# Performance work log

Measured on AMD Instinct MI355X. Metric: run time of the kernel, lower is better.

Reference implementation:

```python
import jax, jax.numpy as jnp
import numpy as np

N = 128   # n_features == out_dim (required by the Christoffel permutes)
H = 256   # MLP hidden width of forward_func
B = 16    # batch size (state_batch is [2B, N])
EPS_G = 1e-4
EPS_DG = 1e-6
EPS_V = 1e-6


def setup_inputs() -> dict:
    key = jax.random.key(0)
    ks = jax.random.split(key, 6)
    return {
        "t": jax.random.uniform(ks[0], (), dtype=jnp.float32),
        "state_batch": jax.random.normal(ks[1], (2 * B, N), dtype=jnp.float32) * 0.1,
        "x0_batch": jax.random.normal(ks[2], (B, N), dtype=jnp.float32),
        "x1_batch": jax.random.normal(ks[3], (B, N), dtype=jnp.float32),
        "W1": jax.random.normal(ks[4], (N, H), dtype=jnp.float32) / np.float32(np.sqrt(N)),
        "b1": jnp.zeros((H,), dtype=jnp.float32),
        "W2": jax.random.normal(ks[5], (H, N), dtype=jnp.float32) / np.float32(np.sqrt(H)),
        "b2": jnp.zeros((N,), dtype=jnp.float32),
    }


def reference(t, state_batch, x0_batch, x1_batch, W1, b1, W2, b2):
    def f(x):  # forward_func, per-sample: [N] -> [N]
        return jnp.tanh(x @ W1 + b1) @ W2 + b2

    def metric(x):  # G(x) = J J^T + 1e-4 I, per-sample: [N] -> [N, N]
        J = jax.jacrev(f)(x)                      # [N, N], matches per-output grad loop
        return J @ J.T + EPS_G * jnp.eye(N, dtype=x.dtype)

    deviation, dev_velocity = jnp.split(state_batch, 2, axis=0)  # each [B, N]
    window = 4.0 * t * (1.0 - t)
    # x along the perturbed straight path
    x = x0_batch + t * (x1_batch - x0_batch) + window * deviation  # [B, N]

    # dG[b, i, j, k] = dG_ij/dx_k -- replaces the out_dim^2 autograd.grad loop
    dG = jax.vmap(jax.jacfwd(metric))(x)  # [B, N, N, N]
    nrm = jnp.sqrt(jnp.sum(dG * dG, axis=(1, 2, 3), keepdims=True))
    dG = dG / (nrm + EPS_DG)

    # Christoffel-like symbols
    Gamma = 0.5 * (dG + jnp.transpose(dG, (0, 2, 1, 3)) - jnp.transpose(dG, (0, 3, 1, 2)))
    a = -jnp.einsum('bijk,bj,bk->bi', Gamma, dev_velocity, dev_velocity)
    a = a / (jnp.linalg.norm(dev_velocity, axis=1, keepdims=True) + EPS_V)

    restoration = -0.1 * deviation
    return jnp.concatenate([dev_velocity, a + restoration], axis=0)  # [2B, N]
```

## Files before the change

### kernel.cpp

```cpp
#include <hip/hip_runtime.h>
#include <math.h>


static constexpr int OFF_W2T  = 0;
static constexpr int OFF_S    = 32768;
static constexpr int OFF_Q    = 98304;
static constexpr int OFF_D    = 163840;
static constexpr int OFF_C    = 167936;
static constexpr int OFF_UV   = 172032;
static constexpr int OFF_AV   = 176128;
static constexpr int OFF_VN   = 180224;
static constexpr int OFF_SUM  = 180240;
static constexpr int OFF_CNT  = 180256;
static constexpr int OFF_PT   = 180288;
static constexpr int OFF_PN   = 704576;

__global__ __launch_bounds__(256) void k_stage1(const float* __restrict__ tptr,
                                                const float* __restrict__ state,
                                                const float* __restrict__ x0,
                                                const float* __restrict__ x1,
                                                const float* __restrict__ W1,
                                                const float* __restrict__ b1,
                                                const float* __restrict__ W2,
                                                float* __restrict__ ws,
                                                float* __restrict__ out) {
    __shared__ __align__(16) float smem[2 * 32 * 34];
    int blk = blockIdx.x;
    int tid = threadIdx.x;

    if (blk < 64) {
        float* Ai = smem;
        float* Aj = smem + 1088;
        int m0 = (blk >> 3) * 32, n0 = (blk & 7) * 32;
        int lx = tid & 31, lr = tid >> 5;
        int tx = tid & 15, ty = tid >> 4;
        float a00 = 0, a01 = 0, a10 = 0, a11 = 0;
        for (int kc = 0; kc < 128; kc += 32) {
            #pragma unroll
            for (int i = 0; i < 4; ++i) {
                int k = lr + 8 * i;
                Ai[k * 34 + lx] = W1[(kc + k) * 256 + m0 + lx];
                Aj[k * 34 + lx] = W1[(kc + k) * 256 + n0 + lx];
            }
            __syncthreads();
            #pragma unroll
            for (int k = 0; k < 32; ++k) {
                float2 a = *(const float2*)&Ai[k * 34 + 2 * ty];
                float2 b = *(const float2*)&Aj[k * 34 + 2 * tx];
                a00 += a.x * b.x; a01 += a.x * b.y;
                a10 += a.y * b.x; a11 += a.y * b.y;
            }
            __syncthreads();
        }
        float* S = ws + OFF_S;
        int m = m0 + 2 * ty, n = n0 + 2 * tx;
        S[m * 256 + n]           = a00;
        S[m * 256 + n + 1]       = a01;
        S[(m + 1) * 256 + n]     = a10;
        S[(m + 1) * 256 + n + 1] = a11;
    } else if (blk < 128) {
        float* Xi = smem;
        float* Xj = smem + 1088;
        int bq = blk - 64;
        int m0 = (bq >> 3) * 32, n0 = (bq & 7) * 32;
        int lx = tid & 31, lr = tid >> 5;
        int tx = tid & 15, ty = tid >> 4;
        float a00 = 0, a01 = 0, a10 = 0, a11 = 0;
        for (int kc = 0; kc < 128; kc += 32) {
            #pragma unroll
            for (int i = 0; i < 4; ++i) {
                Xi[lx * 34 + lr + 8 * i] = W2[(m0 + lr + 8 * i) * 128 + kc + lx];
                Xj[lx * 34 + lr + 8 * i] = W2[(n0 + lr + 8 * i) * 128 + kc + lx];
            }
            __syncthreads();
            #pragma unroll
            for (int k = 0; k < 32; ++k) {
                float2 a = *(const float2*)&Xi[k * 34 + 2 * ty];
                float2 b = *(const float2*)&Xj[k * 34 + 2 * tx];
                a00 += a.x * b.x; a01 += a.x * b.y;
                a10 += a.y * b.x; a11 += a.y * b.y;
            }
            __syncthreads();
        }
        float* Q = ws + OFF_Q;
        int m = m0 + 2 * ty, n = n0 + 2 * tx;
        Q[m * 256 + n]           = a00;
        Q[m * 256 + n + 1]       = a01;
        Q[(m + 1) * 256 + n]     = a10;
        Q[(m + 1) * 256 + n + 1] = a11;
    } else if (blk < 160) {
        float* tile = smem;
        int b2 = blk - 128;
        int c0 = (b2 & 3) * 32, r0 = (b2 >> 2) * 32;
        int tx = tid & 31, ty = tid >> 5;
        #pragma unroll
        for (int i = 0; i < 32; i += 8)
            tile[(ty + i) * 33 + tx] = W2[(r0 + ty + i) * 128 + c0 + tx];
        __syncthreads();
        float* W2T = ws + OFF_W2T;
        #pragma unroll
        for (int i = 0; i < 32; i += 8)
            W2T[(c0 + ty + i) * 256 + r0 + tx] = tile[tx * 33 + ty + i];
    } else {
        int b = blk - 160;
        float* xs  = smem;
        float* vs  = smem + 128;
        float* red = smem + 256;
        float t = tptr[0];
        float w = 4.f * t * (1.f - t);
        if (tid == 0) {
            ws[OFF_SUM + b] = 0.f;
            ((int*)(ws + OFF_CNT))[b] = 0;
        }
        if (tid < 128) {
            float dev = state[b * 128 + tid];
            float v   = state[(16 + b) * 128 + tid];
            float xv  = x0[b * 128 + tid] + t * (x1[b * 128 + tid] - x0[b * 128 + tid]) + w * dev;
            xs[tid] = xv;
            vs[tid] = v;
            out[b * 128 + tid] = v;
            red[tid] = v * v;
        }
        __syncthreads();
        for (int s = 64; s > 0; s >>= 1) {
            if (tid < s) red[tid] += red[tid + s];
            __syncthreads();
        }
        if (tid == 0) ws[OFF_VN + b] = sqrtf(red[0]);

        int m = tid;
        float h = b1[m], uvm = 0.f;
        #pragma unroll 8
        for (int k = 0; k < 128; ++k) {
            float wv = W1[k * 256 + m];
            h   += xs[k] * wv;
            uvm += vs[k] * wv;
        }
        float z  = tanhf(h);
        float dd = 1.f - z * z;
        float cc = -2.f * z * dd;
        const float4* w2r = (const float4*)&W2[m * 128];
        const float4* vs4 = (const float4*)vs;
        float avm = 0.f;
        #pragma unroll 8
        for (int j4 = 0; j4 < 32; ++j4) {
            float4 ww = w2r[j4];
            float4 vv = vs4[j4];
            avm += ww.x * vv.x + ww.y * vv.y + ww.z * vv.z + ww.w * vv.w;
        }
        ws[OFF_D  + b * 256 + m] = dd;
        ws[OFF_C  + b * 256 + m] = cc;
        ws[OFF_UV + b * 256 + m] = uvm;
        ws[OFF_AV + b * 256 + m] = avm;
    }
}

__global__ __launch_bounds__(256) void k_pmat3(const float* __restrict__ Smat,
                                               const float* __restrict__ dall,
                                               const float* __restrict__ W2,
                                               float* __restrict__ PT,
                                               float* __restrict__ Pn) {
    __shared__ __align__(16) float ST[32 * 36];
    __shared__ __align__(16) float YT[32 * 68];
    int b = blockIdx.z, mt = blockIdx.y, jt = blockIdx.x;
    int m0 = mt * 32, j0 = jt * 64;
    const float* dvec = dall + b * 256;
    int tid = threadIdx.x;
    int n = tid >> 3, c4 = (tid & 7) * 4;
    int ty = tid >> 5, tx = tid & 31;
    float acc[4][2] = {};
    for (int nc = 0; nc < 256; nc += 32) {
        *(float4*)&ST[n * 36 + c4] = *(const float4*)&Smat[(nc + n) * 256 + m0 + c4];
        float dn = dvec[nc + n];
        #pragma unroll
        for (int i = 0; i < 2; ++i) {
            int col = c4 + 32 * i;
            float4 wv = *(const float4*)&W2[(nc + n) * 128 + j0 + col];
            wv.x *= dn; wv.y *= dn; wv.z *= dn; wv.w *= dn;
            *(float4*)&YT[n * 68 + col] = wv;
        }
        __syncthreads();
        #pragma unroll 8
        for (int k = 0; k < 32; ++k) {
            float4 a  = *(const float4*)&ST[k * 36 + 4 * ty];
            float2 bb = *(const float2*)&YT[k * 68 + 2 * tx];
            acc[0][0] += a.x * bb.x; acc[0][1] += a.x * bb.y;
            acc[1][0] += a.y * bb.x; acc[1][1] += a.y * bb.y;
            acc[2][0] += a.z * bb.x; acc[2][1] += a.z * bb.y;
            acc[3][0] += a.w * bb.x; acc[3][1] += a.w * bb.y;
        }
        __syncthreads();
    }
    float* ptb = PT + b * 32768;
    float* pnb = Pn + b * 32768;
    #pragma unroll
    for (int jj = 0; jj < 2; ++jj) {
        float4 v = make_float4(acc[0][jj], acc[1][jj], acc[2][jj], acc[3][jj]);
        *(float4*)&ptb[(j0 + 2 * tx + jj) * 256 + m0 + 4 * ty] = v;
    }
    #pragma unroll
    for (int ii = 0; ii < 4; ++ii) {
        float2 v = make_float2(acc[ii][0], acc[ii][1]);
        *(float2*)&pnb[(m0 + 4 * ty + ii) * 128 + j0 + 2 * tx] = v;
    }
}

__global__ __launch_bounds__(256) void k_fnorm3(const float* __restrict__ PT,
                                                const float* __restrict__ Pn,
                                                const float* __restrict__ W2T,
                                                const float* __restrict__ Smat,
                                                const float* __restrict__ Qmat,
                                                const float* __restrict__ state,
                                                const float* __restrict__ W2,
                                                float* __restrict__ ws,
                                                float* __restrict__ out) {
    __shared__ __align__(16) float lds[16384];
    __shared__ int lastflag;
    __shared__ float snrm;
    float* PiT = lds;
    float* PjT = lds + 4096;
    float* WiT = lds + 8192;
    float* WjT = lds + 12288;
    int b = blockIdx.y;
    int idx = blockIdx.x;
    int tj = 0;
    while ((tj + 1) * (tj + 2) / 2 <= idx) ++tj;
    int ti = idx - tj * (tj + 1) / 2;
    int mi0 = ti * 32, mj0 = tj * 32;
    int tid = threadIdx.x;
    const float* ptb = PT + b * 32768;
    int jr = tid >> 3, jc4 = (tid & 7) * 4;
    #pragma unroll
    for (int it = 0; it < 4; ++it) {
        int j = jr + 32 * it;
        *(float4*)&PiT[j * 32 + jc4] = *(const float4*)&ptb[j * 256 + mi0 + jc4];
        *(float4*)&PjT[j * 32 + jc4] = *(const float4*)&ptb[j * 256 + mj0 + jc4];
        *(float4*)&WiT[j * 32 + jc4] = *(const float4*)&W2T[j * 256 + mi0 + jc4];
        *(float4*)&WjT[j * 32 + jc4] = *(const float4*)&W2T[j * 256 + mj0 + jc4];
    }
    __syncthreads();
    int w = tid >> 6, s = tid & 63;
    int ty = s >> 3, tx = s & 7;
    float r[4][4] = {}, f[4][4] = {}, g[4][4] = {};
    int jbase = 32 * w;
    #pragma unroll 4
    for (int jj = 0; jj < 32; ++jj) {
        int j = jbase + jj;
        float4 pi4 = *(const float4*)&PiT[j * 32 + 4 * ty];
        float4 pj4 = *(const float4*)&PjT[j * 32 + 4 * tx];
        float4 wi4 = *(const float4*)&WiT[j * 32 + 4 * ty];
        float4 wj4 = *(const float4*)&WjT[j * 32 + 4 * tx];
        float pi[4] = {pi4.x, pi4.y, pi4.z, pi4.w};
        float pj[4] = {pj4.x, pj4.y, pj4.z, pj4.w};
        float wi[4] = {wi4.x, wi4.y, wi4.z, wi4.w};
        float wj[4] = {wj4.x, wj4.y, wj4.z, wj4.w};
        #pragma unroll
        for (int ii = 0; ii < 4; ++ii)
            #pragma unroll
            for (int kk = 0; kk < 4; ++kk) {
                r[ii][kk] += pi[ii] * pj[kk];
                f[ii][kk] += pi[ii] * wj[kk];
                g[ii][kk] += pj[kk] * wi[ii];
            }
    }
    __syncthreads();
    {
        float* scr = lds;
        int base = tid * 48;
        #pragma unroll
        for (int ii = 0; ii < 4; ++ii)
            #pragma unroll
            for (int kk = 0; kk < 4; ++kk) {
                scr[base + ii * 4 + kk]      = r[ii][kk];
                scr[base + 16 + ii * 4 + kk] = f[ii][kk];
                scr[base + 32 + ii * 4 + kk] = g[ii][kk];
            }
    }
    __syncthreads();
    if (tid < 64) {
        const float* scr = lds;
        float tr[16], tf[16], tg[16];
        #pragma unroll
        for (int k = 0; k < 16; ++k) {
            tr[k] = scr[tid * 48 + k]      + scr[(tid + 64) * 48 + k]
                  + scr[(tid + 128) * 48 + k] + scr[(tid + 192) * 48 + k];
            tf[k] = scr[tid * 48 + 16 + k]      + scr[(tid + 64) * 48 + 16 + k]
                  + scr[(tid + 128) * 48 + 16 + k] + scr[(tid + 192) * 48 + 16 + k];
            tg[k] = scr[tid * 48 + 32 + k]      + scr[(tid + 64) * 48 + 32 + k]
                  + scr[(tid + 128) * 48 + 32 + k] + scr[(tid + 192) * 48 + 32 + k];
        }
        const float* cb = ws + OFF_C + b * 256;
        int mi = mi0 + 4 * (tid >> 3), mj = mj0 + 4 * (tid & 7);
        float4 ce4 = *(const float4*)&cb[mj];
        float ce[4] = {ce4.x, ce4.y, ce4.z, ce4.w};
        float sum = 0.f;
        #pragma unroll
        for (int ii = 0; ii < 4; ++ii) {
            float ci = cb[mi + ii];
            float4 S4 = *(const float4*)&Smat[(mi + ii) * 256 + mj];
            float4 Q4 = *(const float4*)&Qmat[(mi + ii) * 256 + mj];
            float Sv[4] = {S4.x, S4.y, S4.z, S4.w};
            float Qv[4] = {Q4.x, Q4.y, Q4.z, Q4.w};
            #pragma unroll
            for (int kk = 0; kk < 4; ++kk)
                sum += ci * ce[kk] * Sv[kk] * (Qv[kk] * tr[ii * 4 + kk] + tf[ii * 4 + kk] * tg[ii * 4 + kk]);
        }
        if (ti < tj) sum *= 2.f;
        #pragma unroll
        for (int off = 32; off > 0; off >>= 1)
            sum += __shfl_down(sum, off);
        if (tid == 0) {
            atomicAdd(&ws[OFF_SUM + b], sum);
            __threadfence();
            int old = atomicAdd(((int*)(ws + OFF_CNT)) + b, 1);
            lastflag = (old == 35) ? 1 : 0;
        }
    }
    __syncthreads();
    if (!lastflag) return;

    float* vs  = lds;
    float* g1  = lds + 128;
    float* g2  = lds + 384;
    float* red = lds + 640;
    if (tid == 0) {
        float tot = atomicAdd(&ws[OFF_SUM + b], 0.0f);
        snrm = sqrtf(fmaxf(2.f * tot, 0.f));
    }
    if (tid < 128) vs[tid] = state[(16 + b) * 128 + tid];
    __syncthreads();
    const float* pnb = Pn + b * 32768;
    int m = tid;
    float pv = 0.f;
    #pragma unroll 8
    for (int j = 0; j < 128; ++j)
        pv += ptb[j * 256 + m] * vs[j];
    float cc  = ws[OFF_C  + b * 256 + m];
    float uvm = ws[OFF_UV + b * 256 + m];
    float avm = ws[OFF_AV + b * 256 + m];
    g1[m] = cc * pv  * uvm;
    g2[m] = cc * avm * uvm;
    __syncthreads();
    int i = tid & 127, half = tid >> 7;
    int mmlo = half * 128;
    float raw = 0.f;
    #pragma unroll 8
    for (int mm = mmlo; mm < mmlo + 128; ++mm)
        raw += W2[mm * 128 + i] * g1[mm] + pnb[mm * 128 + i] * g2[mm];
    red[tid] = raw;
    __syncthreads();
    if (tid < 128) {
        float rawt = red[tid] + red[tid + 128];
        float vn = ws[OFF_VN + b];
        float a  = -0.5f * rawt / ((snrm + 1e-6f) * (vn + 1e-6f));
        out[(16 + b) * 128 + tid] = a - 0.1f * state[b * 128 + tid];
    }
}

extern "C" void kernel_launch(void* const* d_in, const int* in_sizes, int n_in,
                              void* d_out, int out_size, void* d_ws, size_t ws_size,
                              hipStream_t stream) {
    (void)in_sizes; (void)n_in; (void)out_size; (void)ws_size;
    const float* t     = (const float*)d_in[0];
    const float* state = (const float*)d_in[1];
    const float* x0    = (const float*)d_in[2];
    const float* x1    = (const float*)d_in[3];
    const float* W1    = (const float*)d_in[4];
    const float* b1    = (const float*)d_in[5];
    const float* W2    = (const float*)d_in[6];
    float* out = (float*)d_out;
    float* ws  = (float*)d_ws;

    k_stage1<<<176, 256, 0, stream>>>(t, state, x0, x1, W1, b1, W2, ws, out);
    k_pmat3<<<dim3(2, 8, 16), 256, 0, stream>>>(ws + OFF_S, ws + OFF_D, W2,
                                                ws + OFF_PT, ws + OFF_PN);
    k_fnorm3<<<dim3(36, 16), 256, 0, stream>>>(ws + OFF_PT, ws + OFF_PN, ws + OFF_W2T,
                                               ws + OFF_S, ws + OFF_Q,
                                               state, W2, ws, out);
}
```

Measured before the change: 129.0 us.

## Fuse three kernels into one cooperative persistent kernel with grid syncs

Merges the stage1, pmat and fnorm kernels into a single cooperative kernel of 256 blocks that separates phases with grid.sync. The final per-batch reduction now runs after a grid barrier instead of using atomic counters and a last-block flag. The aim is to remove launch gaps and the inter-kernel boundaries. In exchange, grid barriers cost time, the fnorm tiles are spread over a fixed grid through a strided loop, and all blocks carry the larger LDS footprint. The scratch stride was also padded from 48 to 49 to reduce LDS bank conflicts.

Result: slower. 218.5 us (+69.4%).

```diff
diff --git a/kernel.cpp b/kernel.cpp
--- a/kernel.cpp
+++ b/kernel.cpp
@@ -1,5 +1,8 @@
 #include <hip/hip_runtime.h>
+#include <hip/hip_cooperative_groups.h>
 #include <math.h>
+
+namespace cg = cooperative_groups;
 
 
 static constexpr int OFF_W2T  = 0;
@@ -11,26 +14,27 @@
 static constexpr int OFF_AV   = 176128;
 static constexpr int OFF_VN   = 180224;
 static constexpr int OFF_SUM  = 180240;
-static constexpr int OFF_CNT  = 180256;
-static constexpr int OFF_PT   = 180288;
-static constexpr int OFF_PN   = 704576;
-
-__global__ __launch_bounds__(256) void k_stage1(const float* __restrict__ tptr,
+static constexpr int OFF_PT   = 180256;
+static constexpr int OFF_PN   = OFF_PT + 16 * 32768;
+
+__global__ __launch_bounds__(256, 1) void k_all(const float* __restrict__ tptr,
                                                 const float* __restrict__ state,
                                                 const float* __restrict__ x0,
                                                 const float* __restrict__ x1,
                                                 const float* __restrict__ W1,
                                                 const float* __restrict__ b1,
                                                 const float* __restrict__ W2,
-                                                float* __restrict__ ws,
-                                                float* __restrict__ out) {
-    __shared__ __align__(16) float smem[2 * 32 * 34];
+                                                float* ws,
+                                                float* out) {
+    __shared__ __align__(16) float lds[16384];
+    __shared__ float snrm;
+    cg::grid_group grid = cg::this_grid();
     int blk = blockIdx.x;
     int tid = threadIdx.x;
 
     if (blk < 64) {
-        float* Ai = smem;
-        float* Aj = smem + 1088;
+        float* Ai = lds;
+        float* Aj = lds + 1088;
         int m0 = (blk >> 3) * 32, n0 = (blk & 7) * 32;
         int lx = tid & 31, lr = tid >> 5;
         int tx = tid & 15, ty = tid >> 4;
@@ -59,8 +63,8 @@
         S[(m + 1) * 256 + n]     = a10;
         S[(m + 1) * 256 + n + 1] = a11;
     } else if (blk < 128) {
-        float* Xi = smem;
-        float* Xj = smem + 1088;
+        float* Xi = lds;
+        float* Xj = lds + 1088;
         int bq = blk - 64;
         int m0 = (bq >> 3) * 32, n0 = (bq & 7) * 32;
         int lx = tid & 31, lr = tid >> 5;
@@ -88,30 +92,14 @@
         Q[m * 256 + n + 1]       = a01;
         Q[(m + 1) * 256 + n]     = a10;
         Q[(m + 1) * 256 + n + 1] = a11;
-    } else if (blk < 160) {
-        float* tile = smem;
-        int b2 = blk - 128;
-        int c0 = (b2 & 3) * 32, r0 = (b2 >> 2) * 32;
-        int tx = tid & 31, ty = tid >> 5;
-        #pragma unroll
-        for (int i = 0; i < 32; i += 8)
-            tile[(ty + i) * 33 + tx] = W2[(r0 + ty + i) * 128 + c0 + tx];
-        __syncthreads();
-        float* W2T = ws + OFF_W2T;
-        #pragma unroll
-        for (int i = 0; i < 32; i += 8)
-            W2T[(c0 + ty + i) * 256 + r0 + tx] = tile[tx * 33 + ty + i];
-    } else {
-        int b = blk - 160;
-        float* xs  = smem;
-        float* vs  = smem + 128;
-        float* red = smem + 256;
+    } else if (blk < 144) {
+        int b = blk - 128;
+        float* xs  = lds;
+        float* vs  = lds + 128;
+        float* red = lds + 256;
         float t = tptr[0];
         float w = 4.f * t * (1.f - t);
-        if (tid == 0) {
-            ws[OFF_SUM + b] = 0.f;
-            ((int*)(ws + OFF_CNT))[b] = 0;
-        }
+        if (tid == 0) ws[OFF_SUM + b] = 0.f;
         if (tid < 128) {
             float dev = state[b * 128 + tid];
             float v   = state[(16 + b) * 128 + tid];
@@ -152,208 +140,212 @@
         ws[OFF_C  + b * 256 + m] = cc;
         ws[OFF_UV + b * 256 + m] = uvm;
         ws[OFF_AV + b * 256 + m] = avm;
+    } else if (blk < 160) {
+        float* tile = lds;
+        int tx = tid & 31, ty = tid >> 5;
+        for (int tt = 0; tt < 2; ++tt) {
+            int t2 = (blk - 144) * 2 + tt;
+            int c0 = (t2 & 3) * 32, r0 = (t2 >> 2) * 32;
+            #pragma unroll
+            for (int i = 0; i < 32; i += 8)
+                tile[(ty + i) * 33 + tx] = W2[(r0 + ty + i) * 128 + c0 + tx];
+            __syncthreads();
+            float* W2T = ws + OFF_W2T;
+            #pragma unroll
+            for (int i = 0; i < 32; i += 8)
+                W2T[(c0 + ty + i) * 256 + r0 + tx] = tile[tx * 33 + ty + i];
+            __syncthreads();
+        }
     }
-}
-
-__global__ __launch_bounds__(256) void k_pmat3(const float* __restrict__ Smat,
-                                               const float* __restrict__ dall,
-                                               const float* __restrict__ W2,
-                                               float* __restrict__ PT,
-                                               float* __restrict__ Pn) {
-    __shared__ __align__(16) float ST[32 * 36];
-    __shared__ __align__(16) float YT[32 * 68];
-    int b = blockIdx.z, mt = blockIdx.y, jt = blockIdx.x;
-    int m0 = mt * 32, j0 = jt * 64;
-    const float* dvec = dall + b * 256;
-    int tid = threadIdx.x;
-    int n = tid >> 3, c4 = (tid & 7) * 4;
-    int ty = tid >> 5, tx = tid & 31;
-    float acc[4][2] = {};
-    for (int nc = 0; nc < 256; nc += 32) {
-        *(float4*)&ST[n * 36 + c4] = *(const float4*)&Smat[(nc + n) * 256 + m0 + c4];
-        float dn = dvec[nc + n];
+    grid.sync();
+
+    {
+        float* ST = lds;
+        float* YT = lds + 32 * 36;
+        int b = blk >> 4, rem = blk & 15;
+        int mt = rem >> 1, jt = rem & 1;
+        int m0 = mt * 32, j0 = jt * 64;
+        const float* dvec = ws + OFF_D + b * 256;
+        const float* Smat = ws + OFF_S;
+        int n = tid >> 3, c4 = (tid & 7) * 4;
+        int ty = tid >> 5, tx = tid & 31;
+        float acc[4][2] = {};
+        for (int nc = 0; nc < 256; nc += 32) {
+            *(float4*)&ST[n * 36 + c4] = *(const float4*)&Smat[(nc + n) * 256 + m0 + c4];
+            float dn = dvec[nc + n];
+            #pragma unroll
+            for (int i = 0; i < 2; ++i) {
+                int col = c4 + 32 * i;
+                float4 wv = *(const float4*)&W2[(nc + n) * 128 + j0 + col];
+                wv.x *= dn; wv.y *= dn; wv.z *= dn; wv.w *= dn;
+                *(float4*)&YT[n * 68 + col] = wv;
+            }
+            __syncthreads();
+            #pragma unroll 8
+            for (int k = 0; k < 32; ++k) {
+                float4 a  = *(const float4*)&ST[k * 36 + 4 * ty];
+                float2 bb = *(const float2*)&YT[k * 68 + 2 * tx];
+                acc[0][0] += a.x * bb.x; acc[0][1] += a.x * bb.y;
+                acc[1][0] += a.y * bb.x; acc[1][1] += a.y * bb.y;
+                acc[2][0] += a.z * bb.x; acc[2][1] += a.z * bb.y;
+                acc[3][0] += a.w * bb.x; acc[3][1] += a.w * bb.y;
+            }
+            __syncthreads();
+        }
+        float* ptb = ws + OFF_PT + b * 32768;
+        float* pnb = ws + OFF_PN + b * 32768;
         #pragma unroll
-        for (int i = 0; i < 2; ++i) {
-            int col = c4 + 32 * i;
-            float4 wv = *(const float4*)&W2[(nc + n) * 128 + j0 + col];
-            wv.x *= dn; wv.y *= dn; wv.z *= dn; wv.w *= dn;
-            *(float4*)&YT[n * 68 + col] = wv;
-        }
-        __syncthreads();
-        #pragma unroll 8
-        for (int k = 0; k < 32; ++k) {
-            float4 a  = *(const float4*)&ST[k * 36 + 4 * ty];
-            float2 bb = *(const float2*)&YT[k * 68 + 2 * tx];
-            acc[0][0] += a.x * bb.x; acc[0][1] += a.x * bb.y;
-            acc[1][0] += a.y * bb.x; acc[1][1] += a.y * bb.y;
-            acc[2][0] += a.z * bb.x; acc[2][1] += a.z * bb.y;
-            acc[3][0] += a.w * bb.x; acc[3][1] += a.w * bb.y;
-        }
-        __syncthreads();
-    }
-    float* ptb = PT + b * 32768;
-    float* pnb = Pn + b * 32768;
-    #pragma unroll
-    for (int jj = 0; jj < 2; ++jj) {
-        float4 v = make_float4(acc[0][jj], acc[1][jj], acc[2][jj], acc[3][jj]);
-        *(float4*)&ptb[(j0 + 2 * tx + jj) * 256 + m0 + 4 * ty] = v;
-    }
-    #pragma unroll
-    for (int ii = 0; ii < 4; ++ii) {
-        float2 v = make_float2(acc[ii][0], acc[ii][1]);
-        *(float2*)&pnb[(m0 + 4 * ty + ii) * 128 + j0 + 2 * tx] = v;
-    }
-}
-
-__global__ __launch_bounds__(256) void k_fnorm3(const float* __restrict__ PT,
-                                                const float* __restrict__ Pn,
-                                                const float* __restrict__ W2T,
-                                                const float* __restrict__ Smat,
-                                                const float* __restrict__ Qmat,
-                                                const float* __restrict__ state,
-                                                const float* __restrict__ W2,
-                                                float* __restrict__ ws,
-                                                float* __restrict__ out) {
-    __shared__ __align__(16) float lds[16384];
-    __shared__ int lastflag;
-    __shared__ float snrm;
-    float* PiT = lds;
-    float* PjT = lds + 4096;
-    float* WiT = lds + 8192;
-    float* WjT = lds + 12288;
-    int b = blockIdx.y;
-    int idx = blockIdx.x;
-    int tj = 0;
-    while ((tj + 1) * (tj + 2) / 2 <= idx) ++tj;
-    int ti = idx - tj * (tj + 1) / 2;
-    int mi0 = ti * 32, mj0 = tj * 32;
-    int tid = threadIdx.x;
-    const float* ptb = PT + b * 32768;
-    int jr = tid >> 3, jc4 = (tid & 7) * 4;
-    #pragma unroll
-    for (int it = 0; it < 4; ++it) {
-        int j = jr + 32 * it;
-        *(float4*)&PiT[j * 32 + jc4] = *(const float4*)&ptb[j * 256 + mi0 + jc4];
-        *(float4*)&PjT[j * 32 + jc4] = *(const float4*)&ptb[j * 256 + mj0 + jc4];
-        *(float4*)&WiT[j * 32 + jc4] = *(const float4*)&W2T[j * 256 + mi0 + jc4];
-        *(float4*)&WjT[j * 32 + jc4] = *(const float4*)&W2T[j * 256 + mj0 + jc4];
-    }
-    __syncthreads();
-    int w = tid >> 6, s = tid & 63;
-    int ty = s >> 3, tx = s & 7;
-    float r[4][4] = {}, f[4][4] = {}, g[4][4] = {};
-    int jbase = 32 * w;
-    #pragma unroll 4
-    for (int jj = 0; jj < 32; ++jj) {
-        int j = jbase + jj;
-        float4 pi4 = *(const float4*)&PiT[j * 32 + 4 * ty];
-        float4 pj4 = *(const float4*)&PjT[j * 32 + 4 * tx];
-        float4 wi4 = *(const float4*)&WiT[j * 32 + 4 * ty];
-        float4 wj4 = *(const float4*)&WjT[j * 32 + 4 * tx];
-        float pi[4] = {pi4.x, pi4.y, pi4.z, pi4.w};
-        float pj[4] = {pj4.x, pj4.y, pj4.z, pj4.w};
-        float wi[4] = {wi4.x, wi4.y, wi4.z, wi4.w};
-        float wj[4] = {wj4.x, wj4.y, wj4.z, wj4.w};
-        #pragma unroll
-        for (int ii = 0; ii < 4; ++ii)
-            #pragma unroll
-            for (int kk = 0; kk < 4; ++kk) {
-                r[ii][kk] += pi[ii] * pj[kk];
-                f[ii][kk] += pi[ii] * wj[kk];
-                g[ii][kk] += pj[kk] * wi[ii];
-            }
-    }
-    __syncthreads();
-    {
-        float* scr = lds;
-        int base = tid * 48;
-        #pragma unroll
-        for (int ii = 0; ii < 4; ++ii)
-            #pragma unroll
-            for (int kk = 0; kk < 4; ++kk) {
-                scr[base + ii * 4 + kk]      = r[ii][kk];
-                scr[base + 16 + ii * 4 + kk] = f[ii][kk];
-                scr[base + 32 + ii * 4 + kk] = g[ii][kk];
-            }
-    }
-    __syncthreads();
-    if (tid < 64) {
-        const float* scr = lds;
-        float tr[16], tf[16], tg[16];
-        #pragma unroll
-        for (int k = 0; k < 16; ++k) {
-            tr[k] = scr[tid * 48 + k]      + scr[(tid + 64) * 48 + k]
-                  + scr[(tid + 128) * 48 + k] + scr[(tid + 192) * 48 + k];
-            tf[k] = scr[tid * 48 + 16 + k]      + scr[(tid + 64) * 48 + 16 + k]
-                  + scr[(tid + 128) * 48 + 16 + k] + scr[(tid + 192) * 48 + 16 + k];
-            tg[k] = scr[tid * 48 + 32 + k]      + scr[(tid + 64) * 48 + 32 + k]
-                  + scr[(tid + 128) * 48 + 32 + k] + scr[(tid + 192) * 48 + 32 + k];
-        }
-        const float* cb = ws + OFF_C + b * 256;
-        int mi = mi0 + 4 * (tid >> 3), mj = mj0 + 4 * (tid & 7);
-        float4 ce4 = *(const float4*)&cb[mj];
-        float ce[4] = {ce4.x, ce4.y, ce4.z, ce4.w};
-        float sum = 0.f;
+        for (int jj = 0; jj < 2; ++jj) {
+            float4 v = make_float4(acc[0][jj], acc[1][jj], acc[2][jj], acc[3][jj]);
+            *(float4*)&ptb[(j0 + 2 * tx + jj) * 256 + m0 + 4 * ty] = v;
+        }
         #pragma unroll
         for (int ii = 0; ii < 4; ++ii) {
-            float ci = cb[mi + ii];
-            float4 S4 = *(const float4*)&Smat[(mi + ii) * 256 + mj];
-            float4 Q4 = *(const float4*)&Qmat[(mi + ii) * 256 + mj];
-            float Sv[4] = {S4.x, S4.y, S4.z, S4.w};
-            float Qv[4] = {Q4.x, Q4.y, Q4.z, Q4.w};
-            #pragma unroll
-            for (int kk = 0; kk < 4; ++kk)
-                sum += ci * ce[kk] * Sv[kk] * (Qv[kk] * tr[ii * 4 + kk] + tf[ii * 4 + kk] * tg[ii * 4 + kk]);
-        }
-        if (ti < tj) sum *= 2.f;
+            float2 v = make_float2(acc[ii][0], acc[ii][1]);
+            *(float2*)&pnb[(m0 + 4 * ty + ii) * 128 + j0 + 2 * tx] = v;
+        }
+    }
+    grid.sync();
+
+    for (int u = blk; u < 576; u += 256) {
+        int b = u / 36, idx = u - b * 36;
+        int tj = 0;
+        while ((tj + 1) * (tj + 2) / 2 <= idx) ++tj;
+        int ti = idx - tj * (tj + 1) / 2;
+        int mi0 = ti * 32, mj0 = tj * 32;
+        float* PiT = lds;
+        float* PjT = lds + 4096;
+        float* WiT = lds + 8192;
+        float* WjT = lds + 12288;
+        const float* ptb = ws + OFF_PT + b * 32768;
+        const float* W2T = ws + OFF_W2T;
+        int jr = tid >> 3, jc4 = (tid & 7) * 4;
         #pragma unroll
-        for (int off = 32; off > 0; off >>= 1)
-            sum += __shfl_down(sum, off);
+        for (int it = 0; it < 4; ++it) {
+            int j = jr + 32 * it;
+            *(float4*)&PiT[j * 32 + jc4] = *(const float4*)&ptb[j * 256 + mi0 + jc4];
+            *(float4*)&PjT[j * 32 + jc4] = *(const float4*)&ptb[j * 256 + mj0 + jc4];
+            *(float4*)&WiT[j * 32 + jc4] = *(const float4*)&W2T[j * 256 + mi0 + jc4];
+            *(float4*)&WjT[j * 32 + jc4] = *(const float4*)&W2T[j * 256 + mj0 + jc4];
+        }
+        __syncthreads();
+        int w = tid >> 6, s = tid & 63;
+        int ty = s >> 3, tx = s & 7;
+        float r[4][4] = {}, f[4][4] = {}, g[4][4] = {};
+        int jbase = 32 * w;
+        #pragma unroll 4
+        for (int jj = 0; jj < 32; ++jj) {
+            int j = jbase + jj;
+            float4 pi4 = *(const float4*)&PiT[j * 32 + 4 * ty];
+            float4 pj4 = *(const float4*)&PjT[j * 32 + 4 * tx];
+            float4 wi4 = *(const float4*)&WiT[j * 32 + 4 * ty];
+            float4 wj4 = *(const float4*)&WjT[j * 32 + 4 * tx];
+            float pi[4] = {pi4.x, pi4.y, pi4.z, pi4.w};
+            float pj[4] = {pj4.x, pj4.y, pj4.z, pj4.w};
+            float wi[4] = {wi4.x, wi4.y, wi4.z, wi4.w};
+            float wj[4] = {wj4.x, wj4.y, wj4.z, wj4.w};
+            #pragma unroll
+            for (int ii = 0; ii < 4; ++ii)
+                #pragma unroll
+                for (int kk = 0; kk < 4; ++kk) {
+                    r[ii][kk] += pi[ii] * pj[kk];
+                    f[ii][kk] += pi[ii] * wj[kk];
+                    g[ii][kk] += pj[kk] * wi[ii];
+                }
+        }
+        __syncthreads();
+        {
+            float* scr = lds;
+            int base = tid * 49;
+            #pragma unroll
+            for (int ii = 0; ii < 4; ++ii)
+                #pragma unroll
+                for (int kk = 0; kk < 4; ++kk) {
+                    scr[base + ii * 4 + kk]      = r[ii][kk];
+                    scr[base + 16 + ii * 4 + kk] = f[ii][kk];
+                    scr[base + 32 + ii * 4 + kk] = g[ii][kk];
+                }
+        }
+        __syncthreads();
+        if (tid < 64) {
+            const float* scr = lds;
+            float tr[16], tf[16], tg[16];
+            #pragma unroll
+            for (int k = 0; k < 16; ++k) {
+                tr[k] = scr[tid * 49 + k]           + scr[(tid + 64) * 49 + k]
+                      + scr[(tid + 128) * 49 + k]   + scr[(tid + 192) * 49 + k];
+                tf[k] = scr[tid * 49 + 16 + k]      + scr[(tid + 64) * 49 + 16 + k]
+                      + scr[(tid + 128) * 49 + 16 + k] + scr[(tid + 192) * 49 + 16 + k];
+                tg[k] = scr[tid * 49 + 32 + k]      + scr[(tid + 64) * 49 + 32 + k]
+                      + scr[(tid + 128) * 49 + 32 + k] + scr[(tid + 192) * 49 + 32 + k];
+            }
+            const float* cb = ws + OFF_C + b * 256;
+            const float* Smat = ws + OFF_S;
+            const float* Qmat = ws + OFF_Q;
+            int mi = mi0 + 4 * (tid >> 3), mj = mj0 + 4 * (tid & 7);
+            float4 ce4 = *(const float4*)&cb[mj];
+            float ce[4] = {ce4.x, ce4.y, ce4.z, ce4.w};
+            float sum = 0.f;
+            #pragma unroll
+            for (int ii = 0; ii < 4; ++ii) {
+                float ci = cb[mi + ii];
+                float4 S4 = *(const float4*)&Smat[(mi + ii) * 256 + mj];
+                float4 Q4 = *(const float4*)&Qmat[(mi + ii) * 256 + mj];
+                float Sv[4] = {S4.x, S4.y, S4.z, S4.w};
+                float Qv[4] = {Q4.x, Q4.y, Q4.z, Q4.w};
+                #pragma unroll
+                for (int kk = 0; kk < 4; ++kk)
+                    sum += ci * ce[kk] * Sv[kk] * (Qv[kk] * tr[ii * 4 + kk] + tf[ii * 4 + kk] * tg[ii * 4 + kk]);
+            }
+            if (ti < tj) sum *= 2.f;
+            #pragma unroll
+            for (int off = 32; off > 0; off >>= 1)
+                sum += __shfl_down(sum, off);
+            if (tid == 0) atomicAdd(&ws[OFF_SUM + b], sum);
+        }
+        __syncthreads();
+    }
+    grid.sync();
+
+    if (blk < 16) {
+        int b = blk;
+        float* vs  = lds;
+        float* g1  = lds + 128;
+        float* g2  = lds + 384;
+        float* red = lds + 640;
         if (tid == 0) {
-            atomicAdd(&ws[OFF_SUM + b], sum);
-            __threadfence();
-            int old = atomicAdd(((int*)(ws + OFF_CNT)) + b, 1);
-            lastflag = (old == 35) ? 1 : 0;
-        }
-    }
-    __syncthreads();
-    if (!lastflag) return;
-
-    float* vs  = lds;
-    float* g1  = lds + 128;
-    float* g2  = lds + 384;
-    float* red = lds + 640;
-    if (tid == 0) {
-        float tot = atomicAdd(&ws[OFF_SUM + b], 0.0f);
-        snrm = sqrtf(fmaxf(2.f * tot, 0.f));
-    }
-    if (tid < 128) vs[tid] = state[(16 + b) * 128 + tid];
-    __syncthreads();
-    const float* pnb = Pn + b * 32768;
-    int m = tid;
-    float pv = 0.f;
-    #pragma unroll 8
-    for (int j = 0; j < 128; ++j)
-        pv += ptb[j * 256 + m] * vs[j];
-    float cc  = ws[OFF_C  + b * 256 + m];
-    float uvm = ws[OFF_UV + b * 256 + m];
-    float avm = ws[OFF_AV + b * 256 + m];
-    g1[m] = cc * pv  * uvm;
-    g2[m] = cc * avm * uvm;
-    __syncthreads();
-    int i = tid & 127, half = tid >> 7;
-    int mmlo = half * 128;
-    float raw = 0.f;
-    #pragma unroll 8
-    for (int mm = mmlo; mm < mmlo + 128; ++mm)
-        raw += W2[mm * 128 + i] * g1[mm] + pnb[mm * 128 + i] * g2[mm];
-    red[tid] = raw;
-    __syncthreads();
-    if (tid < 128) {
-        float rawt = red[tid] + red[tid + 128];
-        float vn = ws[OFF_VN + b];
-        float a  = -0.5f * rawt / ((snrm + 1e-6f) * (vn + 1e-6f));
-        out[(16 + b) * 128 + tid] = a - 0.1f * state[b * 128 + tid];
+            float tot = atomicAdd(&ws[OFF_SUM + b], 0.0f);
+            snrm = sqrtf(fmaxf(2.f * tot, 0.f));
+        }
+        if (tid < 128) vs[tid] = state[(16 + b) * 128 + tid];
+        __syncthreads();
+        const float* ptb = ws + OFF_PT + b * 32768;
+        const float* pnb = ws + OFF_PN + b * 32768;
+        int m = tid;
+        float pv = 0.f;
+        #pragma unroll 8
+        for (int j = 0; j < 128; ++j)
+            pv += ptb[j * 256 + m] * vs[j];
+        float cc  = ws[OFF_C  + b * 256 + m];
+        float uvm = ws[OFF_UV + b * 256 + m];
+        float avm = ws[OFF_AV + b * 256 + m];
+        g1[m] = cc * pv  * uvm;
+        g2[m] = cc * avm * uvm;
+        __syncthreads();
+        int i = tid & 127, half = tid >> 7;
+        int mmlo = half * 128;
+        float raw = 0.f;
+        #pragma unroll 8
+        for (int mm = mmlo; mm < mmlo + 128; ++mm)
+            raw += W2[mm * 128 + i] * g1[mm] + pnb[mm * 128 + i] * g2[mm];
+        red[tid] = raw;
+        __syncthreads();
+        if (tid < 128) {
+            float rawt = red[tid] + red[tid + 128];
+            float vn = ws[OFF_VN + b];
+            float a  = -0.5f * rawt / ((snrm + 1e-6f) * (vn + 1e-6f));
+            out[(16 + b) * 128 + tid] = a - 0.1f * state[b * 128 + tid];
+        }
     }
 }
 
@@ -371,10 +363,7 @@
     float* out = (float*)d_out;
     float* ws  = (float*)d_ws;
 
-    k_stage1<<<176, 256, 0, stream>>>(t, state, x0, x1, W1, b1, W2, ws, out);
-    k_pmat3<<<dim3(2, 8, 16), 256, 0, stream>>>(ws + OFF_S, ws + OFF_D, W2,
-                                                ws + OFF_PT, ws + OFF_PN);
-    k_fnorm3<<<dim3(36, 16), 256, 0, stream>>>(ws + OFF_PT, ws + OFF_PN, ws + OFF_W2T,
-                                               ws + OFF_S, ws + OFF_Q,
-                                               state, W2, ws, out);
+    void* args[] = {(void*)&t, (void*)&state, (void*)&x0, (void*)&x1,
+                    (void*)&W1, (void*)&b1, (void*)&W2, (void*)&ws, (void*)&out};
+    hipLaunchCooperativeKernel((const void*)k_all, dim3(256), dim3(256), args, 0, stream);
 }
```

## Split fnorm into many small wave-sized blocks plus separate finalize kernel

Applied to the files above, without the earlier changes.

Replaces the 576-block, 256-thread norm kernel, which staged four panels in LDS and reduced per-thread partials through LDS, with 1152 single-wavefront blocks that stream PT and W2T straight from global memory and accumulate in registers. The last-block-done counter is removed. The final acceleration computation moves into its own 16-block kernel, and the duplicate Pn matrix is no longer written; the finalize step reads PT rows instead. The aim is more parallelism and less LDS and sync overhead, at the cost of an extra kernel launch, redundant uncached global loads and non-coalesced row reads in the finalize step.

New measurement: 171.9 us. 1.33x slower.

```diff
diff --git a/kernel.cpp b/kernel.cpp
--- a/kernel.cpp
+++ b/kernel.cpp
@@ -11,9 +11,7 @@
 static constexpr int OFF_AV   = 176128;
 static constexpr int OFF_VN   = 180224;
 static constexpr int OFF_SUM  = 180240;
-static constexpr int OFF_CNT  = 180256;
-static constexpr int OFF_PT   = 180288;
-static constexpr int OFF_PN   = 704576;
+static constexpr int OFF_PT   = 180256;
 
 __global__ __launch_bounds__(256) void k_stage1(const float* __restrict__ tptr,
                                                 const float* __restrict__ state,
@@ -108,10 +106,7 @@
         float* red = smem + 256;
         float t = tptr[0];
         float w = 4.f * t * (1.f - t);
-        if (tid == 0) {
-            ws[OFF_SUM + b] = 0.f;
-            ((int*)(ws + OFF_CNT))[b] = 0;
-        }
+        if (tid == 0) ws[OFF_SUM + b] = 0.f;
         if (tid < 128) {
             float dev = state[b * 128 + tid];
             float v   = state[(16 + b) * 128 + tid];
@@ -158,8 +153,7 @@
 __global__ __launch_bounds__(256) void k_pmat3(const float* __restrict__ Smat,
                                                const float* __restrict__ dall,
                                                const float* __restrict__ W2,
-                                               float* __restrict__ PT,
-                                               float* __restrict__ Pn) {
+                                               float* __restrict__ PT) {
     __shared__ __align__(16) float ST[32 * 36];
     __shared__ __align__(16) float YT[32 * 68];
     int b = blockIdx.z, mt = blockIdx.y, jt = blockIdx.x;
@@ -192,144 +186,84 @@
         __syncthreads();
     }
     float* ptb = PT + b * 32768;
-    float* pnb = Pn + b * 32768;
     #pragma unroll
     for (int jj = 0; jj < 2; ++jj) {
         float4 v = make_float4(acc[0][jj], acc[1][jj], acc[2][jj], acc[3][jj]);
         *(float4*)&ptb[(j0 + 2 * tx + jj) * 256 + m0 + 4 * ty] = v;
     }
-    #pragma unroll
-    for (int ii = 0; ii < 4; ++ii) {
-        float2 v = make_float2(acc[ii][0], acc[ii][1]);
-        *(float2*)&pnb[(m0 + 4 * ty + ii) * 128 + j0 + 2 * tx] = v;
-    }
-}
-
-__global__ __launch_bounds__(256) void k_fnorm3(const float* __restrict__ PT,
-                                                const float* __restrict__ Pn,
-                                                const float* __restrict__ W2T,
-                                                const float* __restrict__ Smat,
-                                                const float* __restrict__ Qmat,
-                                                const float* __restrict__ state,
-                                                const float* __restrict__ W2,
-                                                float* __restrict__ ws,
-                                                float* __restrict__ out) {
-    __shared__ __align__(16) float lds[16384];
-    __shared__ int lastflag;
-    __shared__ float snrm;
-    float* PiT = lds;
-    float* PjT = lds + 4096;
-    float* WiT = lds + 8192;
-    float* WjT = lds + 12288;
-    int b = blockIdx.y;
-    int idx = blockIdx.x;
+}
+
+__global__ __launch_bounds__(64) void k_fnorm4(const float* __restrict__ PT,
+                                               const float* __restrict__ W2T,
+                                               const float* __restrict__ Smat,
+                                               const float* __restrict__ Qmat,
+                                               const float* __restrict__ call,
+                                               float* __restrict__ sums) {
+    int task = blockIdx.x;
+    int u = task >> 1, h = task & 1;
+    int b = u / 36, idx = u - b * 36;
     int tj = 0;
     while ((tj + 1) * (tj + 2) / 2 <= idx) ++tj;
     int ti = idx - tj * (tj + 1) / 2;
-    int mi0 = ti * 32, mj0 = tj * 32;
     int tid = threadIdx.x;
+    int ty = tid >> 4, tx = tid & 15;
+    int mi = ti * 32 + h * 16 + 4 * ty;
+    int mj = tj * 32 + 2 * tx;
     const float* ptb = PT + b * 32768;
-    int jr = tid >> 3, jc4 = (tid & 7) * 4;
-    #pragma unroll
-    for (int it = 0; it < 4; ++it) {
-        int j = jr + 32 * it;
-        *(float4*)&PiT[j * 32 + jc4] = *(const float4*)&ptb[j * 256 + mi0 + jc4];
-        *(float4*)&PjT[j * 32 + jc4] = *(const float4*)&ptb[j * 256 + mj0 + jc4];
-        *(float4*)&WiT[j * 32 + jc4] = *(const float4*)&W2T[j * 256 + mi0 + jc4];
-        *(float4*)&WjT[j * 32 + jc4] = *(const float4*)&W2T[j * 256 + mj0 + jc4];
-    }
-    __syncthreads();
-    int w = tid >> 6, s = tid & 63;
-    int ty = s >> 3, tx = s & 7;
-    float r[4][4] = {}, f[4][4] = {}, g[4][4] = {};
-    int jbase = 32 * w;
+    const float* pir = ptb + mi;
+    const float* pjr = ptb + mj;
+    const float* wir = W2T + mi;
+    const float* wjr = W2T + mj;
+    float r[4][2] = {}, f[4][2] = {}, g[4][2] = {};
     #pragma unroll 4
-    for (int jj = 0; jj < 32; ++jj) {
-        int j = jbase + jj;
-        float4 pi4 = *(const float4*)&PiT[j * 32 + 4 * ty];
-        float4 pj4 = *(const float4*)&PjT[j * 32 + 4 * tx];
-        float4 wi4 = *(const float4*)&WiT[j * 32 + 4 * ty];
-        float4 wj4 = *(const float4*)&WjT[j * 32 + 4 * tx];
-        float pi[4] = {pi4.x, pi4.y, pi4.z, pi4.w};
-        float pj[4] = {pj4.x, pj4.y, pj4.z, pj4.w};
-        float wi[4] = {wi4.x, wi4.y, wi4.z, wi4.w};
-        float wj[4] = {wj4.x, wj4.y, wj4.z, wj4.w};
-        #pragma unroll
-        for (int ii = 0; ii < 4; ++ii)
-            #pragma unroll
-            for (int kk = 0; kk < 4; ++kk) {
-                r[ii][kk] += pi[ii] * pj[kk];
-                f[ii][kk] += pi[ii] * wj[kk];
-                g[ii][kk] += pj[kk] * wi[ii];
-            }
-    }
-    __syncthreads();
-    {
-        float* scr = lds;
-        int base = tid * 48;
-        #pragma unroll
-        for (int ii = 0; ii < 4; ++ii)
-            #pragma unroll
-            for (int kk = 0; kk < 4; ++kk) {
-                scr[base + ii * 4 + kk]      = r[ii][kk];
-                scr[base + 16 + ii * 4 + kk] = f[ii][kk];
-                scr[base + 32 + ii * 4 + kk] = g[ii][kk];
-            }
-    }
-    __syncthreads();
-    if (tid < 64) {
-        const float* scr = lds;
-        float tr[16], tf[16], tg[16];
-        #pragma unroll
-        for (int k = 0; k < 16; ++k) {
-            tr[k] = scr[tid * 48 + k]      + scr[(tid + 64) * 48 + k]
-                  + scr[(tid + 128) * 48 + k] + scr[(tid + 192) * 48 + k];
-            tf[k] = scr[tid * 48 + 16 + k]      + scr[(tid + 64) * 48 + 16 + k]
-                  + scr[(tid + 128) * 48 + 16 + k] + scr[(tid + 192) * 48 + 16 + k];
-            tg[k] = scr[tid * 48 + 32 + k]      + scr[(tid + 64) * 48 + 32 + k]
-                  + scr[(tid + 128) * 48 + 32 + k] + scr[(tid + 192) * 48 + 32 + k];
-        }
-        const float* cb = ws + OFF_C + b * 256;
-        int mi = mi0 + 4 * (tid >> 3), mj = mj0 + 4 * (tid & 7);
-        float4 ce4 = *(const float4*)&cb[mj];
-        float ce[4] = {ce4.x, ce4.y, ce4.z, ce4.w};
-        float sum = 0.f;
+    for (int j = 0; j < 128; ++j) {
+        float4 pi = *(const float4*)&pir[j * 256];
+        float2 pj = *(const float2*)&pjr[j * 256];
+        float4 wi = *(const float4*)&wir[j * 256];
+        float2 wj = *(const float2*)&wjr[j * 256];
+        float pia[4] = {pi.x, pi.y, pi.z, pi.w};
+        float wia[4] = {wi.x, wi.y, wi.z, wi.w};
         #pragma unroll
         for (int ii = 0; ii < 4; ++ii) {
-            float ci = cb[mi + ii];
-            float4 S4 = *(const float4*)&Smat[(mi + ii) * 256 + mj];
-            float4 Q4 = *(const float4*)&Qmat[(mi + ii) * 256 + mj];
-            float Sv[4] = {S4.x, S4.y, S4.z, S4.w};
-            float Qv[4] = {Q4.x, Q4.y, Q4.z, Q4.w};
-            #pragma unroll
-            for (int kk = 0; kk < 4; ++kk)
-                sum += ci * ce[kk] * Sv[kk] * (Qv[kk] * tr[ii * 4 + kk] + tf[ii * 4 + kk] * tg[ii * 4 + kk]);
-        }
-        if (ti < tj) sum *= 2.f;
-        #pragma unroll
-        for (int off = 32; off > 0; off >>= 1)
-            sum += __shfl_down(sum, off);
-        if (tid == 0) {
-            atomicAdd(&ws[OFF_SUM + b], sum);
-            __threadfence();
-            int old = atomicAdd(((int*)(ws + OFF_CNT)) + b, 1);
-            lastflag = (old == 35) ? 1 : 0;
-        }
-    }
-    __syncthreads();
-    if (!lastflag) return;
-
-    float* vs  = lds;
-    float* g1  = lds + 128;
-    float* g2  = lds + 384;
-    float* red = lds + 640;
+            r[ii][0] += pia[ii] * pj.x;  r[ii][1] += pia[ii] * pj.y;
+            f[ii][0] += pia[ii] * wj.x;  f[ii][1] += pia[ii] * wj.y;
+            g[ii][0] += pj.x * wia[ii];  g[ii][1] += pj.y * wia[ii];
+        }
+    }
+    const float* cb = call + b * 256;
+    float2 ce = *(const float2*)&cb[mj];
+    float sum = 0.f;
+    #pragma unroll
+    for (int ii = 0; ii < 4; ++ii) {
+        float ci = cb[mi + ii];
+        float2 S2 = *(const float2*)&Smat[(mi + ii) * 256 + mj];
+        float2 Q2 = *(const float2*)&Qmat[(mi + ii) * 256 + mj];
+        sum += ci * ce.x * S2.x * (Q2.x * r[ii][0] + f[ii][0] * g[ii][0]);
+        sum += ci * ce.y * S2.y * (Q2.y * r[ii][1] + f[ii][1] * g[ii][1]);
+    }
+    if (ti < tj) sum *= 2.f;
+    #pragma unroll
+    for (int off = 32; off > 0; off >>= 1)
+        sum += __shfl_down(sum, off);
+    if (tid == 0) atomicAdd(&sums[b], sum);
+}
+
+__global__ __launch_bounds__(256) void k_fin3(const float* __restrict__ state,
+                                              const float* __restrict__ W2,
+                                              float* __restrict__ ws,
+                                              float* __restrict__ out) {
+    int b = blockIdx.x;
+    int tid = threadIdx.x;
+    __shared__ float vs[128], g1[256], g2[256], red[256];
+    __shared__ float snrm;
+    if (tid < 128) vs[tid] = state[(16 + b) * 128 + tid];
     if (tid == 0) {
         float tot = atomicAdd(&ws[OFF_SUM + b], 0.0f);
         snrm = sqrtf(fmaxf(2.f * tot, 0.f));
     }
-    if (tid < 128) vs[tid] = state[(16 + b) * 128 + tid];
     __syncthreads();
-    const float* pnb = Pn + b * 32768;
+
+    const float* ptb = ws + OFF_PT + b * 32768;
     int m = tid;
     float pv = 0.f;
     #pragma unroll 8
@@ -341,12 +275,14 @@
     g1[m] = cc * pv  * uvm;
     g2[m] = cc * avm * uvm;
     __syncthreads();
+
     int i = tid & 127, half = tid >> 7;
     int mmlo = half * 128;
+    const float* ptrow = ptb + i * 256;
     float raw = 0.f;
     #pragma unroll 8
     for (int mm = mmlo; mm < mmlo + 128; ++mm)
-        raw += W2[mm * 128 + i] * g1[mm] + pnb[mm * 128 + i] * g2[mm];
+        raw += W2[mm * 128 + i] * g1[mm] + ptrow[mm] * g2[mm];
     red[tid] = raw;
     __syncthreads();
     if (tid < 128) {
@@ -372,9 +308,8 @@
     float* ws  = (float*)d_ws;
 
     k_stage1<<<176, 256, 0, stream>>>(t, state, x0, x1, W1, b1, W2, ws, out);
-    k_pmat3<<<dim3(2, 8, 16), 256, 0, stream>>>(ws + OFF_S, ws + OFF_D, W2,
-                                                ws + OFF_PT, ws + OFF_PN);
-    k_fnorm3<<<dim3(36, 16), 256, 0, stream>>>(ws + OFF_PT, ws + OFF_PN, ws + OFF_W2T,
-                                               ws + OFF_S, ws + OFF_Q,
-                                               state, W2, ws, out);
-}
+    k_pmat3<<<dim3(2, 8, 16), 256, 0, stream>>>(ws + OFF_S, ws + OFF_D, W2, ws + OFF_PT);
+    k_fnorm4<<<1152, 64, 0, stream>>>(ws + OFF_PT, ws + OFF_W2T, ws + OFF_S,
+                                      ws + OFF_Q, ws + OFF_C, ws + OFF_SUM);
+    k_fin3<<<16, 256, 0, stream>>>(state, W2, ws, out);
+}
```
